# Performance work log

Hardware: AMD Instinct MI355X
Metric: run time of the kernel (lower is better)

The kernel has to match this reference:

```python
import jax, jax.numpy as jnp
import numpy as np
from jax import lax

D = 1024      # dim
E = 2         # expand
DI = D * E    # d_inner = 2048
DS = 16       # d_state
DK = 3        # d_conv (3 so padding=1 preserves seq length)
DTR = 64      # dt_rank = ceil(dim/16)
B = 2
L = 4096


def setup_inputs() -> dict:
    key = jax.random.key(0)
    ks = jax.random.split(key, 8)
    s = 0.02
    return {
        "x": jax.random.normal(ks[0], (B, L, D), jnp.float32),
        "W_in": jax.random.normal(ks[1], (D, 2 * DI), jnp.float32) * s,
        "W_conv": jax.random.normal(ks[2], (DI, 1, DK), jnp.float32) * s,
        "W_xproj": jax.random.normal(ks[3], (DI, DTR + 2 * DS), jnp.float32) * s,
        "W_dt": jax.random.normal(ks[4], (DTR, DI), jnp.float32) * s,
        "b_dt": jax.random.normal(ks[5], (DI,), jnp.float32) * s,
        "W_out": jax.random.normal(ks[6], (DI, D), jnp.float32) * s,
        "ln_g": jnp.ones((DI,), jnp.float32),
        "ln_b": jnp.zeros((DI,), jnp.float32),
    }


def _silu(v):
    return v * jax.nn.sigmoid(v)


def _forward(x, W_in, W_conv, W_xproj, W_dt, b_dt, W_out, ln_g, ln_b):
    # in_proj and gate split
    xz = x @ W_in                                   # (B,L,2*DI)
    xs, z = jnp.split(xz, 2, axis=-1)               # (B,L,DI) each
    # depthwise conv1d (groups = DI), padding preserves L
    xc = lax.conv_general_dilated(
        xs.transpose(0, 2, 1), W_conv, (1,), [(DK // 2, DK // 2)],
        dimension_numbers=("NCH", "OIH", "NCH"), feature_group_count=DI)
    xs = _silu(xc.transpose(0, 2, 1))               # (B,L,DI)
    # x_proj -> dt, B, C
    xp = xs @ W_xproj                               # (B,L,DTR+2*DS)
    dt_lo = xp[..., :DTR]
    Bp = xp[..., DTR:DTR + DS]                      # (B,L,DS)
    Cp = xp[..., DTR + DS:]                         # (B,L,DS)
    dt = jax.nn.softplus(dt_lo @ W_dt + b_dt)       # (B,L,DI)
    # simplified selective scan: scalar decay/input per (b,t)
    dtm = dt.mean(-1)                               # (B,L)
    xm = xs.mean(-1)                                # (B,L)
    decay = jnp.exp(-dtm)                           # (B,L)
    Bx = Bp * xm[..., None]                         # (B,L,DS)

    def step(h, inp):
        d, bx = inp                                 # d:(B,), bx:(B,DS)
        h = h * d[:, None] + bx
        return h, h.sum(-1)                         # emit sum_s h[b,s]

    h0 = jnp.zeros((x.shape[0], DS), x.dtype)
    _, S = lax.scan(step, h0, (decay.T, Bx.transpose(1, 0, 2)))  # S:(L,B)
    y = Cp * S.T[..., None]                         # (B,L,DS): y_t = C_t * sum_s h_t
    y = jnp.tile(y, (1, 1, DI // DS))               # broadcast up to d_inner
    # LayerNorm(d_inner)
    mu = y.mean(-1, keepdims=True)
    var = y.var(-1, keepdims=True)
    y = (y - mu) * lax.rsqrt(var + 1e-5) * ln_g + ln_b
    # gate and out_proj
    y = y * _silu(z)
    return y @ W_out                                # (B,L,D)


def reference(x, W_in, W_conv, W_xproj, W_dt, b_dt, W_out, ln_g, ln_b):
    return _forward(x, W_in, W_conv, W_xproj, W_dt, b_dt, W_out, ln_g, ln_b)
```

## Files before the change

kernel.cpp:

```cpp
#include <hip/hip_runtime.h>
#include <hip/hip_bf16.h>
#include <math.h>
#include <stdint.h>

#define D_    1024
#define DI_   2048
#define DS_   16
#define DTR_  64
#define B_    2
#define L_    4096
#define ROWS_ 8192
#define NXZ_  4096

typedef __attribute__((ext_vector_type(8))) __bf16 bf16x8;
typedef __attribute__((ext_vector_type(4))) float  f32x4;

__device__ __forceinline__ unsigned short f2bf(float f) {
    unsigned u = __float_as_uint(f);
    unsigned r = (u + 0x7fffu + ((u >> 16) & 1u)) >> 16;
    return (unsigned short)r;
}
__device__ __forceinline__ float bf2f(unsigned short h) {
    return __uint_as_float(((unsigned)h) << 16);
}

__device__ __forceinline__ void gload16(const void* gp, void* lp) {
    auto* g1 = (const __attribute__((address_space(1))) unsigned int*)(uintptr_t)gp;
    auto* l3 = (__attribute__((address_space(3))) unsigned int*)(uintptr_t)lp;
    __builtin_amdgcn_global_load_lds(g1, l3, 16, 0, 0);
}

__global__ __launch_bounds__(256) void kcvt(const float* __restrict__ in,
                                            unsigned short* __restrict__ out) {
    const int i = blockIdx.x * 256 + threadIdx.x;
    const float4 v = ((const float4*)in)[i];
    ushort4 o;
    o.x = f2bf(v.x); o.y = f2bf(v.y); o.z = f2bf(v.z); o.w = f2bf(v.w);
    ((ushort4*)out)[i] = o;
}

__global__ __launch_bounds__(256) void ktrans(const float* __restrict__ W,
                                              unsigned short* __restrict__ WT,
                                              int R, int Csrc) {
    __shared__ float tile[32][33];
    const int c0 = blockIdx.x * 32, r0 = blockIdx.y * 32;
    const int tc = threadIdx.x & 31, tr = threadIdx.x >> 5;
#pragma unroll
    for (int i = 0; i < 32; i += 8)
        tile[tr + i][tc] = (c0 + tc < Csrc)
                           ? W[(size_t)(r0 + tr + i) * Csrc + c0 + tc] : 0.f;
    __syncthreads();
#pragma unroll
    for (int i = 0; i < 32; i += 8)
        WT[(size_t)(c0 + tr + i) * R + r0 + tc] = f2bf(tile[tc][tr + i]);
}

template <int K, bool BF16OUT>
__global__ __launch_bounds__(512, 2) void gemm256b(const unsigned short* __restrict__ A,
                                                   const unsigned short* __restrict__ Bm,
                                                   void* __restrict__ Cp, int ldc) {
    constexpr int NT = K / 64;
    const int t = threadIdx.x;
    const int wid = t >> 6, lane = t & 63;
    const int l15 = lane & 15, g = lane >> 4;
    const int gx = gridDim.x, nwg = gx * gridDim.y;
    int lin = blockIdx.y * gx + blockIdx.x;
    lin = (lin & 7) * (nwg >> 3) + (lin >> 3);
    const int m0 = (lin % gx) * 256;
    const int n0 = (lin / gx) * 128;
    const int wr = wid >> 1, wc = wid & 1;

    __shared__ unsigned short lds[49152];

    int pr[2], ps[2];
#pragma unroll
    for (int j = 0; j < 2; ++j) {
        const int p = (wid * 2 + j) * 64 + lane;
        pr[j] = p >> 3;
        ps[j] = (p & 7) ^ (pr[j] & 7);
    }
    auto stage = [&](int kt, int which) {
        if (kt >= NT) return;
        const int buf = kt & 1;
        const unsigned short* src = (which == 2) ? Bm : A;
        const int row0 = (which == 2) ? n0 : (m0 + ((which == 1) ? 128 : 0));
        const int base_byte = buf * 49152 + which * 16384;
#pragma unroll
        for (int j = 0; j < 2; ++j)
            gload16(src + (size_t)(row0 + pr[j]) * K + kt * 64 + ps[j] * 8,
                    (char*)lds + base_byte + (wid * 2 + j) * 1024);
    };
    auto lda = [&](int buf, int m, int kk) -> bf16x8 {
        const int R = wr * 64 + m * 16 + l15;
        const int S = kk * 4 + g;
        return *(const bf16x8*)&lds[buf * 24576 + R * 64 + ((S ^ (l15 & 7)) << 3)];
    };
    auto ldb = [&](int buf, int n, int kk) -> bf16x8 {
        const int R = wc * 64 + n * 16 + l15;
        const int S = kk * 4 + g;
        return *(const bf16x8*)&lds[buf * 24576 + 16384 + R * 64 + ((S ^ (l15 & 7)) << 3)];
    };

    f32x4 acc[4][4];
    const f32x4 z4 = {0.f, 0.f, 0.f, 0.f};
#pragma unroll
    for (int m = 0; m < 4; ++m)
#pragma unroll
        for (int n = 0; n < 4; ++n) acc[m][n] = z4;
    bf16x8 a[2][2], b[4][2];

    stage(0, 0); stage(0, 1); stage(0, 2); stage(1, 0);
    asm volatile("s_waitcnt vmcnt(2)" ::: "memory");
    __builtin_amdgcn_s_barrier();

    for (int it = 0; it < NT; ++it) {
        const int buf = it & 1;
#pragma unroll
        for (int m = 0; m < 2; ++m) { a[m][0] = lda(buf, m, 0); a[m][1] = lda(buf, m, 1); }
#pragma unroll
        for (int n = 0; n < 2; ++n) { b[n][0] = ldb(buf, n, 0); b[n][1] = ldb(buf, n, 1); }
        stage(it + 1, 1);
        __builtin_amdgcn_s_barrier();
        __builtin_amdgcn_s_setprio(1);
#pragma unroll
        for (int m = 0; m < 2; ++m)
#pragma unroll
            for (int n = 0; n < 2; ++n)
#pragma unroll
                for (int kk = 0; kk < 2; ++kk)
                    acc[m][n] = __builtin_amdgcn_mfma_f32_16x16x32_bf16(
                        a[m][kk], b[n][kk], acc[m][n], 0, 0, 0);
        __builtin_amdgcn_s_setprio(0);
        __builtin_amdgcn_s_barrier();
#pragma unroll
        for (int n = 2; n < 4; ++n) { b[n][0] = ldb(buf, n, 0); b[n][1] = ldb(buf, n, 1); }
        stage(it + 1, 2);
        __builtin_amdgcn_s_barrier();
        __builtin_amdgcn_s_setprio(1);
#pragma unroll
        for (int m = 0; m < 2; ++m)
#pragma unroll
            for (int n = 2; n < 4; ++n)
#pragma unroll
                for (int kk = 0; kk < 2; ++kk)
                    acc[m][n] = __builtin_amdgcn_mfma_f32_16x16x32_bf16(
                        a[m][kk], b[n][kk], acc[m][n], 0, 0, 0);
        __builtin_amdgcn_s_setprio(0);
        __builtin_amdgcn_s_barrier();
#pragma unroll
        for (int m = 0; m < 2; ++m) { a[m][0] = lda(buf, 2 + m, 0); a[m][1] = lda(buf, 2 + m, 1); }
        __builtin_amdgcn_s_barrier();
        __builtin_amdgcn_s_setprio(1);
#pragma unroll
        for (int m = 0; m < 2; ++m)
#pragma unroll
            for (int n = 0; n < 2; ++n)
#pragma unroll
                for (int kk = 0; kk < 2; ++kk)
                    acc[2 + m][n] = __builtin_amdgcn_mfma_f32_16x16x32_bf16(
                        a[m][kk], b[n][kk], acc[2 + m][n], 0, 0, 0);
        __builtin_amdgcn_s_setprio(0);
        __builtin_amdgcn_s_barrier();
        stage(it + 2, 0);
        if (it < NT - 2)       { asm volatile("s_waitcnt vmcnt(2)" ::: "memory"); }
        else if (it == NT - 2) { asm volatile("s_waitcnt vmcnt(0)" ::: "memory"); }
        __builtin_amdgcn_s_barrier();
        __builtin_amdgcn_s_setprio(1);
#pragma unroll
        for (int m = 0; m < 2; ++m)
#pragma unroll
            for (int n = 2; n < 4; ++n)
#pragma unroll
                for (int kk = 0; kk < 2; ++kk)
                    acc[2 + m][n] = __builtin_amdgcn_mfma_f32_16x16x32_bf16(
                        a[m][kk], b[n][kk], acc[2 + m][n], 0, 0, 0);
        __builtin_amdgcn_s_setprio(0);
        __builtin_amdgcn_s_barrier();
    }

    const int crow = g * 4;
#pragma unroll
    for (int m = 0; m < 4; ++m)
#pragma unroll
        for (int n = 0; n < 4; ++n)
#pragma unroll
            for (int j = 0; j < 4; ++j) {
                const size_t idx = (size_t)(m0 + wr * 64 + m * 16 + crow + j) * ldc +
                                   (n0 + wc * 64 + n * 16 + l15);
                if (BF16OUT) ((unsigned short*)Cp)[idx] = f2bf(acc[m][n][j]);
                else         ((float*)Cp)[idx] = acc[m][n][j];
            }
}

__global__ __launch_bounds__(256) void k2_conv(const unsigned short* __restrict__ xz,
                                               const float* __restrict__ Wcv,
                                               unsigned short* __restrict__ xsb,
                                               float* __restrict__ xm) {
    const int t = threadIdx.x;
    const int wid = t >> 6, lane = t & 63;
    const int row0 = blockIdx.x * 16;
    const int c0 = t * 8;
    __shared__ float wsum[16][4];
    float w0[8], w1[8], w2[8];
#pragma unroll
    for (int j = 0; j < 8; ++j) {
        w0[j] = Wcv[(c0 + j) * 3 + 0];
        w1[j] = Wcv[(c0 + j) * 3 + 1];
        w2[j] = Wcv[(c0 + j) * 3 + 2];
    }
    for (int r = 0; r < 16; ++r) {
        const int row = row0 + r;
        const int l = row & (L_ - 1);
        const unsigned short* cur = xz + (size_t)row * NXZ_ + c0;
        float cv[8], pv[8] = {}, nv[8] = {};
        {
            const uint4 raw = *(const uint4*)cur;
            const unsigned short* p = (const unsigned short*)&raw;
#pragma unroll
            for (int j = 0; j < 8; ++j) cv[j] = bf2f(p[j]);
        }
        if (l > 0) {
            const uint4 raw = *(const uint4*)(cur - NXZ_);
            const unsigned short* p = (const unsigned short*)&raw;
#pragma unroll
            for (int j = 0; j < 8; ++j) pv[j] = bf2f(p[j]);
        }
        if (l < L_ - 1) {
            const uint4 raw = *(const uint4*)(cur + NXZ_);
            const unsigned short* p = (const unsigned short*)&raw;
#pragma unroll
            for (int j = 0; j < 8; ++j) nv[j] = bf2f(p[j]);
        }
        float s8 = 0.f;
        unsigned short o[8];
#pragma unroll
        for (int j = 0; j < 8; ++j) {
            const float v = cv[j] * w1[j] + pv[j] * w0[j] + nv[j] * w2[j];
            const float s = v / (1.f + expf(-v));
            o[j] = f2bf(s);
            s8 += s;
        }
        *(uint4*)(xsb + (size_t)row * DI_ + c0) = *(const uint4*)o;
#pragma unroll
        for (int k = 1; k < 64; k <<= 1) s8 += __shfl_xor(s8, k);
        if (lane == 0) wsum[r][wid] = s8;
    }
    __syncthreads();
    if (t < 16)
        xm[row0 + t] = (wsum[t][0] + wsum[t][1] + wsum[t][2] + wsum[t][3]) * (1.f / (float)DI_);
}

__global__ __launch_bounds__(256, 2) void k3m(const unsigned short* __restrict__ A,
                                              const unsigned short* __restrict__ B,
                                              float* __restrict__ part) {
    const int t = threadIdx.x;
    const int wid = t >> 6, lane = t & 63;
    const int m0 = blockIdx.x * 128;
    const int kc = blockIdx.y;
    const int wr = wid >> 1, wc = wid & 1;
    __shared__ unsigned short Als[128 * 64];
    __shared__ unsigned short Bls[128 * 64];
    f32x4 acc[4][4];
    const f32x4 z4 = {0.f, 0.f, 0.f, 0.f};
#pragma unroll
    for (int m = 0; m < 4; ++m)
#pragma unroll
        for (int n = 0; n < 4; ++n) acc[m][n] = z4;
    int rowA[4], eoff[4];
#pragma unroll
    for (int i = 0; i < 4; ++i) {
        const int c = wid * 256 + i * 64 + lane;
        rowA[i] = c >> 3;
        eoff[i] = (c & 7) * 8;
    }
    const int ar = wr * 64 + (lane & 15);
    const int br = wc * 64 + (lane & 15);
    const int kq = (lane >> 4) * 8;
    const int kbase = kc * 512;
    for (int k0 = kbase; k0 < kbase + 512; k0 += 64) {
#pragma unroll
        for (int i = 0; i < 4; ++i) {
            const int dst = (wid * 4 + i) * 1024;
            gload16(A + (size_t)(m0 + rowA[i]) * DI_ + k0 + eoff[i], (char*)Als + dst);
            gload16(B + (size_t)rowA[i] * DI_ + k0 + eoff[i], (char*)Bls + dst);
        }
        __syncthreads();
        bf16x8 af[4][2], bfr[4][2];
#pragma unroll
        for (int m = 0; m < 4; ++m)
#pragma unroll
            for (int kk = 0; kk < 2; ++kk)
                af[m][kk] = *(const bf16x8*)&Als[(ar + m * 16) * 64 + kk * 32 + kq];
#pragma unroll
        for (int n = 0; n < 4; ++n)
#pragma unroll
            for (int kk = 0; kk < 2; ++kk)
                bfr[n][kk] = *(const bf16x8*)&Bls[(br + n * 16) * 64 + kk * 32 + kq];
#pragma unroll
        for (int m = 0; m < 4; ++m)
#pragma unroll
            for (int n = 0; n < 4; ++n)
#pragma unroll
                for (int kk = 0; kk < 2; ++kk)
                    acc[m][n] = __builtin_amdgcn_mfma_f32_16x16x32_bf16(
                        af[m][kk], bfr[n][kk], acc[m][n], 0, 0, 0);
        __syncthreads();
    }
    const int crow = (lane >> 4) * 4, ccol = lane & 15;
#pragma unroll
    for (int m = 0; m < 4; ++m)
#pragma unroll
        for (int n = 0; n < 4; ++n) {
            const int col = wc * 64 + n * 16 + ccol;
            if (col < 96) {
#pragma unroll
                for (int j = 0; j < 4; ++j)
                    part[((size_t)kc * ROWS_ + m0 + wr * 64 + m * 16 + crow + j) * 96 + col] =
                        acc[m][n][j];
            }
        }
}

__global__ __launch_bounds__(256) void kred(const float* __restrict__ part,
                                            float* __restrict__ xp,
                                            unsigned short* __restrict__ dtlo) {
    const int i = blockIdx.x * 256 + threadIdx.x;
    const size_t stride = (size_t)ROWS_ * 96 / 4;
    const float4* p = (const float4*)part;
    float4 a = p[i], b = p[i + stride], c = p[i + 2 * stride], d = p[i + 3 * stride];
    float4 o;
    o.x = a.x + b.x + c.x + d.x;
    o.y = a.y + b.y + c.y + d.y;
    o.z = a.z + b.z + c.z + d.z;
    o.w = a.w + b.w + c.w + d.w;
    ((float4*)xp)[i] = o;
    const int c4 = i % 24, row = i / 24;
    if (c4 < 16) {
        ushort4 h;
        h.x = f2bf(o.x); h.y = f2bf(o.y); h.z = f2bf(o.z); h.w = f2bf(o.w);
        *(ushort4*)(dtlo + (size_t)row * 64 + c4 * 4) = h;
    }
}

__global__ __launch_bounds__(256, 2) void k4m(const unsigned short* __restrict__ A,
                                              const unsigned short* __restrict__ B,
                                              const float* __restrict__ bdt,
                                              float* __restrict__ psum) {
    const int t = threadIdx.x;
    const int wid = t >> 6, lane = t & 63;
    const int m0 = blockIdx.x * 128;
    const int nb = blockIdx.y;
    const int wr = wid >> 1, wc = wid & 1;
    __shared__ unsigned short Als[128 * 64];
    __shared__ unsigned short Bls[128 * 64];
    __shared__ float srow[128][2];
    f32x4 acc[4][4];
    const f32x4 z4 = {0.f, 0.f, 0.f, 0.f};
#pragma unroll
    for (int m = 0; m < 4; ++m)
#pragma unroll
        for (int n = 0; n < 4; ++n) acc[m][n] = z4;
#pragma unroll
    for (int i = 0; i < 4; ++i) {
        const int c = wid * 256 + i * 64 + lane;
        const int row = c >> 3, eo = (c & 7) * 8;
        const int dst = (wid * 4 + i) * 1024;
        gload16(A + (size_t)(m0 + row) * 64 + eo, (char*)Als + dst);
        gload16(B + (size_t)(nb * 128 + row) * 64 + eo, (char*)Bls + dst);
    }
    __syncthreads();
    const int ar = wr * 64 + (lane & 15);
    const int br = wc * 64 + (lane & 15);
    const int kq = (lane >> 4) * 8;
    const int ccol = lane & 15;
    {
        bf16x8 af[4][2], bfr[4][2];
#pragma unroll
        for (int m = 0; m < 4; ++m)
#pragma unroll
            for (int kk = 0; kk < 2; ++kk)
                af[m][kk] = *(const bf16x8*)&Als[(ar + m * 16) * 64 + kk * 32 + kq];
#pragma unroll
        for (int n = 0; n < 4; ++n)
#pragma unroll
            for (int kk = 0; kk < 2; ++kk)
                bfr[n][kk] = *(const bf16x8*)&Bls[(br + n * 16) * 64 + kk * 32 + kq];
#pragma unroll
        for (int m = 0; m < 4; ++m)
#pragma unroll
            for (int n = 0; n < 4; ++n)
#pragma unroll
                for (int kk = 0; kk < 2; ++kk)
                    acc[m][n] = __builtin_amdgcn_mfma_f32_16x16x32_bf16(
                        af[m][kk], bfr[n][kk], acc[m][n], 0, 0, 0);
    }
    float bcol[4];
#pragma unroll
    for (int n = 0; n < 4; ++n) bcol[n] = bdt[nb * 128 + wc * 64 + n * 16 + ccol];
#pragma unroll
    for (int m = 0; m < 4; ++m)
#pragma unroll
        for (int j = 0; j < 4; ++j) {
            float s = 0.f;
#pragma unroll
            for (int n = 0; n < 4; ++n) {
                const float w = acc[m][n][j] + bcol[n];
                s += fmaxf(w, 0.f) + log1pf(expf(-fabsf(w)));
            }
#pragma unroll
            for (int mask = 1; mask < 16; mask <<= 1) s += __shfl_xor(s, mask);
            if (ccol == 0)
                srow[wr * 64 + m * 16 + (lane >> 4) * 4 + j][wc] = s;
        }
    __syncthreads();
    if (t < 128)
        psum[(size_t)nb * ROWS_ + m0 + t] = srow[t][0] + srow[t][1];
}

__global__ __launch_bounds__(256) void k4r(const float* __restrict__ psum,
                                           const float* __restrict__ xp,
                                           const float* __restrict__ xm,
                                           float* __restrict__ dec,
                                           float* __restrict__ u) {
    const int row = blockIdx.x * 256 + threadIdx.x;
    float tot = 0.f;
#pragma unroll
    for (int j = 0; j < 16; ++j) tot += psum[(size_t)j * ROWS_ + row];
    const float dtm = tot * (1.f / (float)DI_);
    float sBp = 0.f;
#pragma unroll
    for (int s = 0; s < DS_; ++s) sBp += xp[(size_t)row * 96 + DTR_ + s];
    dec[row] = expf(-dtm);
    u[row]   = xm[row] * sBp;
}

__global__ __launch_bounds__(256) void k5_scan(const float* __restrict__ dec,
                                               const float* __restrict__ u,
                                               float* __restrict__ S) {
    const int t = threadIdx.x;
    __shared__ float aa[256], hh[256], init[256];
    const int b = t >> 7, c = t & 127;
    const int base = b * L_ + c * 32;
    float a = 1.f, h = 0.f;
    for (int i = 0; i < 32; ++i) {
        const float d = dec[base + i];
        h = h * d + u[base + i];
        a *= d;
    }
    aa[t] = a; hh[t] = h;
    __syncthreads();
    if (t < B_) {
        float run = 0.f;
        for (int cc = 0; cc < 128; ++cc) {
            const int tt = t * 128 + cc;
            init[tt] = run;
            run = hh[tt] + aa[tt] * run;
        }
    }
    __syncthreads();
    h = init[t];
    for (int i = 0; i < 32; ++i) {
        h = h * dec[base + i] + u[base + i];
        S[base + i] = h;
    }
}

__global__ __launch_bounds__(256) void k6_v16(const float* __restrict__ xp,
                                              const float* __restrict__ S,
                                              float* __restrict__ v16) {
    const int row = blockIdx.x * 256 + threadIdx.x;
    const float s = S[row];
    float v[16], mu = 0.f;
#pragma unroll
    for (int i = 0; i < 16; ++i) {
        v[i] = xp[(size_t)row * 96 + DTR_ + DS_ + i] * s;
        mu += v[i];
    }
    mu *= (1.f / 16.f);
    float var = 0.f;
#pragma unroll
    for (int i = 0; i < 16; ++i) {
        const float d = v[i] - mu;
        var += d * d;
    }
    var *= (1.f / 16.f);
    const float rs = rsqrtf(var + 1e-5f);
#pragma unroll
    for (int i = 0; i < 16; ++i) v16[(size_t)row * 16 + i] = (v[i] - mu) * rs;
}

__global__ __launch_bounds__(256) void kA7(const unsigned short* __restrict__ xz,
                                           const float* __restrict__ v16,
                                           const float* __restrict__ g,
                                           const float* __restrict__ bb,
                                           unsigned short* __restrict__ Abf) {
    const int row = blockIdx.x;
    const int t   = threadIdx.x;
    __shared__ float vrow[16];
    if (t < 16) vrow[t] = v16[row * 16 + t];
    __syncthreads();
    const int i0 = t * 8;
    const uint4 zraw = *(const uint4*)(xz + (size_t)row * NXZ_ + 2048 + i0);
    const unsigned short* zp = (const unsigned short*)&zraw;
    const float4 g0 = *(const float4*)(g + i0),  g1 = *(const float4*)(g + i0 + 4);
    const float4 b0 = *(const float4*)(bb + i0), b1 = *(const float4*)(bb + i0 + 4);
    const float gv[8] = {g0.x, g0.y, g0.z, g0.w, g1.x, g1.y, g1.z, g1.w};
    const float bv[8] = {b0.x, b0.y, b0.z, b0.w, b1.x, b1.y, b1.z, b1.w};
    unsigned short o[8];
#pragma unroll
    for (int j = 0; j < 8; ++j) {
        const int i = i0 + j;
        const float zf = bf2f(zp[j]);
        const float sz = zf / (1.f + expf(-zf));
        o[j] = f2bf((vrow[i & 15] * gv[j] + bv[j]) * sz);
    }
    *(uint4*)(Abf + (size_t)row * DI_ + i0) = *(const uint4*)o;
}

extern "C" void kernel_launch(void* const* d_in, const int* in_sizes, int n_in,
                              void* d_out, int out_size, void* d_ws, size_t ws_size,
                              hipStream_t stream) {
    const float* x    = (const float*)d_in[0];
    const float* Win  = (const float*)d_in[1];
    const float* Wcv  = (const float*)d_in[2];
    const float* Wxp  = (const float*)d_in[3];
    const float* Wdt  = (const float*)d_in[4];
    const float* bdt  = (const float*)d_in[5];
    const float* Wout = (const float*)d_in[6];
    const float* lng  = (const float*)d_in[7];
    const float* lnb  = (const float*)d_in[8];
    float* out = (float*)d_out;

    char* base = (char*)d_ws;
    unsigned short* xz_bf   = (unsigned short*)(base + 0);
    unsigned short* xsb     = (unsigned short*)(base + 67108864);
    unsigned short* xbf     = (unsigned short*)(base + 100663296);
    unsigned short* Abf     = (unsigned short*)(base + 100663296);
    unsigned short* WoutT   = (unsigned short*)(base + 134217728);
    unsigned short* WinT    = (unsigned short*)(base + 138412032);
    unsigned short* WxpT    = (unsigned short*)(base + 146800640);
    unsigned short* WdtT    = (unsigned short*)(base + 147324928);
    float*          xp_part = (float*)(base + 147587072);
    float*          xp      = (float*)(base + 160169984);
    unsigned short* dtlo    = (unsigned short*)(base + 163315712);
    float*          psum    = (float*)(base + 164364288);
    float*          xm      = (float*)(base + 164888576);
    float*          dec     = (float*)(base + 164921344);
    float*          u       = (float*)(base + 164954112);
    float*          S       = (float*)(base + 164986880);
    float*          v16     = (float*)(base + 165019648);

    kcvt<<<ROWS_ * D_ / 1024, 256, 0, stream>>>(x, xbf);
    ktrans<<<dim3(NXZ_ / 32, D_ / 32), 256, 0, stream>>>(Win, WinT, D_, NXZ_);
    ktrans<<<dim3(4, DI_ / 32), 256, 0, stream>>>(Wxp, WxpT, DI_, 96);
    ktrans<<<dim3(DI_ / 32, DTR_ / 32), 256, 0, stream>>>(Wdt, WdtT, DTR_, DI_);
    gemm256b<D_, true><<<dim3(ROWS_ / 256, NXZ_ / 128), 512, 0, stream>>>(
        xbf, WinT, xz_bf, NXZ_);
    ktrans<<<dim3(D_ / 32, DI_ / 32), 256, 0, stream>>>(Wout, WoutT, DI_, D_);
    k2_conv<<<ROWS_ / 16, 256, 0, stream>>>(xz_bf, Wcv, xsb, xm);
    k3m<<<dim3(ROWS_ / 128, 4), 256, 0, stream>>>(xsb, WxpT, xp_part);
    kred<<<ROWS_ * 96 / 4 / 256, 256, 0, stream>>>(xp_part, xp, dtlo);
    k4m<<<dim3(ROWS_ / 128, DI_ / 128), 256, 0, stream>>>(dtlo, WdtT, bdt, psum);
    k4r<<<ROWS_ / 256, 256, 0, stream>>>(psum, xp, xm, dec, u);
    k5_scan<<<1, 256, 0, stream>>>(dec, u, S);
    k6_v16<<<ROWS_ / 256, 256, 0, stream>>>(xp, S, v16);
    kA7<<<ROWS_, 256, 0, stream>>>(xz_bf, v16, lng, lnb, Abf);
    gemm256b<DI_, false><<<dim3(ROWS_ / 256, D_ / 128), 512, 0, stream>>>(
        Abf, WoutT, out, D_);
}
```

Measured before the change: 394.6 us.

## Triple-buffer LDS in bf16 GEMM and merge MFMA phases to cut barriers

```diff
diff --git a/kernel.cpp b/kernel.cpp
--- a/kernel.cpp
+++ b/kernel.cpp
@@ -70,7 +70,7 @@
     const int n0 = (lin / gx) * 128;
     const int wr = wid >> 1, wc = wid & 1;
 
-    __shared__ unsigned short lds[49152];
+    __shared__ unsigned short lds[73728];
 
     int pr[2], ps[2];
 #pragma unroll
@@ -81,7 +81,7 @@
     }
     auto stage = [&](int kt, int which) {
         if (kt >= NT) return;
-        const int buf = kt & 1;
+        const int buf = kt % 3;
         const unsigned short* src = (which == 2) ? Bm : A;
         const int row0 = (which == 2) ? n0 : (m0 + ((which == 1) ? 128 : 0));
         const int base_byte = buf * 49152 + which * 16384;
@@ -109,23 +109,25 @@
         for (int n = 0; n < 4; ++n) acc[m][n] = z4;
     bf16x8 a[2][2], b[4][2];
 
-    stage(0, 0); stage(0, 1); stage(0, 2); stage(1, 0);
-    asm volatile("s_waitcnt vmcnt(2)" ::: "memory");
+    stage(0, 0); stage(0, 1); stage(0, 2);
+    stage(1, 0); stage(1, 1); stage(1, 2);
+    asm volatile("s_waitcnt vmcnt(6)" ::: "memory");
     __builtin_amdgcn_s_barrier();
 
     for (int it = 0; it < NT; ++it) {
-        const int buf = it & 1;
+        const int buf = it % 3;
 #pragma unroll
         for (int m = 0; m < 2; ++m) { a[m][0] = lda(buf, m, 0); a[m][1] = lda(buf, m, 1); }
 #pragma unroll
-        for (int n = 0; n < 2; ++n) { b[n][0] = ldb(buf, n, 0); b[n][1] = ldb(buf, n, 1); }
-        stage(it + 1, 1);
+        for (int n = 0; n < 4; ++n) { b[n][0] = ldb(buf, n, 0); b[n][1] = ldb(buf, n, 1); }
+        stage(it + 2, 1);
+        stage(it + 2, 2);
         __builtin_amdgcn_s_barrier();
         __builtin_amdgcn_s_setprio(1);
 #pragma unroll
         for (int m = 0; m < 2; ++m)
 #pragma unroll
-            for (int n = 0; n < 2; ++n)
+            for (int n = 0; n < 4; ++n)
 #pragma unroll
                 for (int kk = 0; kk < 2; ++kk)
                     acc[m][n] = __builtin_amdgcn_mfma_f32_16x16x32_bf16(
@@ -133,43 +135,16 @@
         __builtin_amdgcn_s_setprio(0);
         __builtin_amdgcn_s_barrier();
 #pragma unroll
-        for (int n = 2; n < 4; ++n) { b[n][0] = ldb(buf, n, 0); b[n][1] = ldb(buf, n, 1); }
-        stage(it + 1, 2);
-        __builtin_amdgcn_s_barrier();
-        __builtin_amdgcn_s_setprio(1);
-#pragma unroll
-        for (int m = 0; m < 2; ++m)
-#pragma unroll
-            for (int n = 2; n < 4; ++n)
-#pragma unroll
-                for (int kk = 0; kk < 2; ++kk)
-                    acc[m][n] = __builtin_amdgcn_mfma_f32_16x16x32_bf16(
-                        a[m][kk], b[n][kk], acc[m][n], 0, 0, 0);
-        __builtin_amdgcn_s_setprio(0);
-        __builtin_amdgcn_s_barrier();
-#pragma unroll
         for (int m = 0; m < 2; ++m) { a[m][0] = lda(buf, 2 + m, 0); a[m][1] = lda(buf, 2 + m, 1); }
-        __builtin_amdgcn_s_barrier();
-        __builtin_amdgcn_s_setprio(1);
-#pragma unroll
-        for (int m = 0; m < 2; ++m)
-#pragma unroll
-            for (int n = 0; n < 2; ++n)
-#pragma unroll
-                for (int kk = 0; kk < 2; ++kk)
-                    acc[2 + m][n] = __builtin_amdgcn_mfma_f32_16x16x32_bf16(
-                        a[m][kk], b[n][kk], acc[2 + m][n], 0, 0, 0);
-        __builtin_amdgcn_s_setprio(0);
-        __builtin_amdgcn_s_barrier();
         stage(it + 2, 0);
-        if (it < NT - 2)       { asm volatile("s_waitcnt vmcnt(2)" ::: "memory"); }
+        if (it < NT - 2)       { asm volatile("s_waitcnt vmcnt(6)" ::: "memory"); }
         else if (it == NT - 2) { asm volatile("s_waitcnt vmcnt(0)" ::: "memory"); }
         __builtin_amdgcn_s_barrier();
         __builtin_amdgcn_s_setprio(1);
 #pragma unroll
         for (int m = 0; m < 2; ++m)
 #pragma unroll
-            for (int n = 2; n < 4; ++n)
+            for (int n = 0; n < 4; ++n)
 #pragma unroll
                 for (int kk = 0; kk < 2; ++kk)
                     acc[2 + m][n] = __builtin_amdgcn_mfma_f32_16x16x32_bf16(
```

Measured after the change: 391.2 us. About the same (-0.9%).
